# Kernel tuning notes

Measured on AMD Instinct MI355X. Metric: run time of the kernel, lower is better.

Reference implementation:

```python
import jax, jax.numpy as jnp
import numpy as np

EMB_DIM = 2048
USER_DIM = 256
NUM_EXPERTS = 64
TOP_K = 8
N_TOKENS = 16384


def setup_inputs() -> dict:
    key = jax.random.key(0)
    k_h, k_u, k_w = jax.random.split(key, 3)
    h = jax.random.normal(k_h, (N_TOKENS, EMB_DIM), dtype=jnp.float32)
    u = jax.random.normal(k_u, (N_TOKENS, USER_DIM), dtype=jnp.float32)
    # nn.Linear weight is [out, in]; we store transposed [in, out] for x @ W
    W = jax.random.normal(k_w, (EMB_DIM + USER_DIM, NUM_EXPERTS), dtype=jnp.float32) * (1.0 / np.sqrt(EMB_DIM + USER_DIM))
    b = jnp.zeros((NUM_EXPERTS,), dtype=jnp.float32)
    return {"h": h, "u": u, "W": W, "b": b}


def reference(h, u, W, b):
    # gate logits: [N, E]
    g = jnp.concatenate([h, u], axis=-1) @ W + b
    w = jax.nn.softmax(g, axis=-1)
    # top-k mask + renormalize (top_k < num_experts)
    _, top_idx = jax.lax.top_k(w, TOP_K)                       # [N, k]
    mask = jax.nn.one_hot(top_idx, NUM_EXPERTS, dtype=w.dtype).sum(axis=-2)  # [N, E]
    w = w * mask
    w = w / (w.sum(axis=-1, keepdims=True) + 1e-9)
    return w
```

## Files before the change

kernel.cpp:

```cpp
#include <hip/hip_runtime.h>

#define EMB 2048
#define UDIM 256
#define KTOT 2304
#define NE 64
#define TOPK 8
#define TPB 64
#define LP 65
#define BK 64
#define NWIN (KTOT / BK)
#define ESL 16

__global__ __launch_bounds__(1024, 4)
void gate_fused(const float* __restrict__ h, const float* __restrict__ u,
                const float* __restrict__ W, const float* __restrict__ b,
                float* __restrict__ out) {
  __shared__ float xt[2][TPB * LP];

  const int tid = threadIdx.x;
  const int lane = tid & 63;
  const int wid = __builtin_amdgcn_readfirstlane(tid >> 6);
  const int kq = wid & 3;
  const int ew = wid >> 2;
  const int tok0 = blockIdx.x * TPB;

  const int stok = tid >> 4;
  const int sseg = (tid & 15) * 4;

  float acc[ESL];
#pragma unroll
  for (int j = 0; j < ESL; ++j) acc[j] = 0.f;

  {
    float4 v = *(const float4*)(h + (size_t)(tok0 + stok) * EMB + sseg);
    float* dst = &xt[0][stok * LP + sseg];
    dst[0] = v.x; dst[1] = v.y; dst[2] = v.z; dst[3] = v.w;
  }
  __syncthreads();

  const int xbase = lane * LP + kq * 16;
  int p = 0;
  for (int w = 0; w < NWIN; ++w) {
    float4 v;
    if (w + 1 < NWIN) {
      const int kn = (w + 1) * BK;
      const float* src = (kn < EMB)
          ? h + (size_t)(tok0 + stok) * EMB + kn + sseg
          : u + (size_t)(tok0 + stok) * UDIM + (kn - EMB) + sseg;
      v = *(const float4*)src;
    }

    const float* wp = W + (size_t)(w * BK + kq * 16) * NE + ew * ESL;
    const float* xp = &xt[p][xbase];

    float4 wc[2][4];
#pragma unroll
    for (int kk = 0; kk < 2; ++kk)
#pragma unroll
      for (int j = 0; j < 4; ++j)
        wc[kk][j] = *(const float4*)(wp + kk * NE + 4 * j);

#pragma unroll
    for (int pr = 0; pr < 8; ++pr) {
      float4 wn[2][4];
      if (pr < 7) {
        const float* wq = wp + (size_t)(2 * pr + 2) * NE;
#pragma unroll
        for (int kk = 0; kk < 2; ++kk)
#pragma unroll
          for (int j = 0; j < 4; ++j)
            wn[kk][j] = *(const float4*)(wq + kk * NE + 4 * j);
      }
      const float x0 = xp[2 * pr];
      const float x1 = xp[2 * pr + 1];
#pragma unroll
      for (int j = 0; j < 4; ++j) {
        acc[4 * j + 0] = __builtin_fmaf(x0, wc[0][j].x, acc[4 * j + 0]);
        acc[4 * j + 1] = __builtin_fmaf(x0, wc[0][j].y, acc[4 * j + 1]);
        acc[4 * j + 2] = __builtin_fmaf(x0, wc[0][j].z, acc[4 * j + 2]);
        acc[4 * j + 3] = __builtin_fmaf(x0, wc[0][j].w, acc[4 * j + 3]);
      }
#pragma unroll
      for (int j = 0; j < 4; ++j) {
        acc[4 * j + 0] = __builtin_fmaf(x1, wc[1][j].x, acc[4 * j + 0]);
        acc[4 * j + 1] = __builtin_fmaf(x1, wc[1][j].y, acc[4 * j + 1]);
        acc[4 * j + 2] = __builtin_fmaf(x1, wc[1][j].z, acc[4 * j + 2]);
        acc[4 * j + 3] = __builtin_fmaf(x1, wc[1][j].w, acc[4 * j + 3]);
      }
      if (pr < 7) {
#pragma unroll
        for (int kk = 0; kk < 2; ++kk)
#pragma unroll
          for (int j = 0; j < 4; ++j) wc[kk][j] = wn[kk][j];
      }
    }

    if (w + 1 < NWIN) {
      float* dst = &xt[1 - p][stok * LP + sseg];
      dst[0] = v.x; dst[1] = v.y; dst[2] = v.z; dst[3] = v.w;
    }
    __syncthreads();
    p ^= 1;
  }

  float* slab = xt[0];
  for (int ph = 0; ph < 4; ++ph) {
    if (kq == ph) {
      float* srow = slab + lane * LP + ew * ESL;
      if (ph == 0) {
#pragma unroll
        for (int j = 0; j < ESL; ++j) srow[j] = acc[j];
      } else {
#pragma unroll
        for (int j = 0; j < ESL; ++j) srow[j] += acc[j];
      }
    }
    __syncthreads();
  }

  const float bias = b[lane];
#pragma unroll
  for (int tt = 0; tt < 4; ++tt) {
    const int t = wid * 4 + tt;
    float g = slab[t * LP + lane] + bias;

    float m = g;
#pragma unroll
    for (int off = 32; off > 0; off >>= 1)
      m = fmaxf(m, __shfl_xor(m, off));
    float pexp = __expf(g - m);
    float s = pexp;
#pragma unroll
    for (int off = 32; off > 0; off >>= 1)
      s += __shfl_xor(s, off);
    const float pn = pexp / s;

    float vv = pn;
    float topsum = 0.f;
    int sel = 0;
    for (int r = 0; r < TOPK; ++r) {
      float mv = vv;
      int mi = lane;
#pragma unroll
      for (int off = 32; off > 0; off >>= 1) {
        const float ov = __shfl_xor(mv, off);
        const int oi = __shfl_xor(mi, off);
        if (ov > mv || (ov == mv && oi < mi)) { mv = ov; mi = oi; }
      }
      topsum += mv;
      if (lane == mi) { sel = 1; vv = -1.f; }
    }

    out[(size_t)(tok0 + t) * NE + lane] =
        sel ? pn / (topsum + 1e-9f) : 0.f;
  }
}

extern "C" void kernel_launch(void* const* d_in, const int* in_sizes, int n_in,
                              void* d_out, int out_size, void* d_ws, size_t ws_size,
                              hipStream_t stream) {
  const float* h = (const float*)d_in[0];
  const float* u = (const float*)d_in[1];
  const float* W = (const float*)d_in[2];
  const float* b = (const float*)d_in[3];
  float* out = (float*)d_out;

  const int n_tokens = in_sizes[0] / EMB;
  const int n_blocks = n_tokens / TPB;

  hipLaunchKernelGGL(gate_fused, dim3(n_blocks), dim3(1024), 0, stream,
                     h, u, W, b, out);
}
```

Before: 293.8 us.

## Replace FP32 FMA gate GEMM with split-bf16 MFMA emulation

```diff
diff --git a/kernel.cpp b/kernel.cpp
--- a/kernel.cpp
+++ b/kernel.cpp
@@ -5,115 +5,138 @@
 #define KTOT 2304
 #define NE 64
 #define TOPK 8
-#define TPB 64
+#define TPB 32
 #define LP 65
-#define BK 64
-#define NWIN (KTOT / BK)
-#define ESL 16
+#define PLANE (KTOT * NE)
 
-__global__ __launch_bounds__(1024, 4)
-void gate_fused(const float* __restrict__ h, const float* __restrict__ u,
-                const float* __restrict__ W, const float* __restrict__ b,
-                float* __restrict__ out) {
-  __shared__ float xt[2][TPB * LP];
+typedef __attribute__((ext_vector_type(8))) short short8;
+typedef __attribute__((ext_vector_type(4))) float f32x4;
+
+__device__ __forceinline__ unsigned short bf16h(float x) {
+  unsigned uu = __builtin_bit_cast(unsigned, x);
+  return (unsigned short)((uu + 0x7FFFu + ((uu >> 16) & 1u)) >> 16);
+}
+__device__ __forceinline__ float bf2f(unsigned short s) {
+  return __builtin_bit_cast(float, ((unsigned)s) << 16);
+}
+
+__global__ __launch_bounds__(256)
+void prep_w(const float* __restrict__ W, unsigned short* __restrict__ wt) {
+  __shared__ unsigned short t0[64][72], t1[64][72], t2[64][72];
+  const int t = threadIdx.x;
+  const int kb = blockIdx.x * 64;
+#pragma unroll
+  for (int i = 0; i < 16; ++i) {
+    const int flat = i * 256 + t;
+    const int kk = flat >> 6;
+    const int nn = flat & 63;
+    const float w = W[(size_t)(kb + kk) * NE + nn];
+    const unsigned short h0 = bf16h(w);
+    const float r1 = w - bf2f(h0);
+    const unsigned short h1 = bf16h(r1);
+    const float r2 = r1 - bf2f(h1);
+    t0[nn][kk] = h0;
+    t1[nn][kk] = h1;
+    t2[nn][kk] = bf16h(r2);
+  }
+  __syncthreads();
+#pragma unroll
+  for (int i = 0; i < 16; ++i) {
+    const int flat = i * 256 + t;
+    const int nn = flat >> 6;
+    const int kk = flat & 63;
+    const size_t idx = (size_t)nn * KTOT + kb + kk;
+    wt[idx] = t0[nn][kk];
+    wt[PLANE + idx] = t1[nn][kk];
+    wt[2 * PLANE + idx] = t2[nn][kk];
+  }
+}
+
+__global__ __launch_bounds__(512, 4)
+void gate_mfma(const float* __restrict__ h, const float* __restrict__ u,
+               const unsigned short* __restrict__ wt,
+               const float* __restrict__ b, float* __restrict__ out) {
+  __shared__ float slab[TPB * LP];
 
   const int tid = threadIdx.x;
   const int lane = tid & 63;
   const int wid = __builtin_amdgcn_readfirstlane(tid >> 6);
-  const int kq = wid & 3;
-  const int ew = wid >> 2;
+  const int tw = wid & 1;
+  const int kq = wid >> 1;
+  const int mm = lane & 15;
+  const int q8 = (lane >> 4) * 8;
   const int tok0 = blockIdx.x * TPB;
+  const int token = tok0 + tw * 16 + mm;
 
-  const int stok = tid >> 4;
-  const int sseg = (tid & 15) * 4;
+  const float* hrow = h + (size_t)token * EMB + q8;
+  const float* urow = u + (size_t)token * UDIM + q8;
+  const unsigned short* wrow[4];
+#pragma unroll
+  for (int nt = 0; nt < 4; ++nt)
+    wrow[nt] = wt + (size_t)(nt * 16 + mm) * KTOT + q8;
 
-  float acc[ESL];
+  f32x4 acc[4];
 #pragma unroll
-  for (int j = 0; j < ESL; ++j) acc[j] = 0.f;
+  for (int nt = 0; nt < 4; ++nt) acc[nt] = 0.f;
 
-  {
-    float4 v = *(const float4*)(h + (size_t)(tok0 + stok) * EMB + sseg);
-    float* dst = &xt[0][stok * LP + sseg];
-    dst[0] = v.x; dst[1] = v.y; dst[2] = v.z; dst[3] = v.w;
-  }
-  __syncthreads();
-
-  const int xbase = lane * LP + kq * 16;
-  int p = 0;
-  for (int w = 0; w < NWIN; ++w) {
-    float4 v;
-    if (w + 1 < NWIN) {
-      const int kn = (w + 1) * BK;
-      const float* src = (kn < EMB)
-          ? h + (size_t)(tok0 + stok) * EMB + kn + sseg
-          : u + (size_t)(tok0 + stok) * UDIM + (kn - EMB) + sseg;
-      v = *(const float4*)src;
-    }
-
-    const float* wp = W + (size_t)(w * BK + kq * 16) * NE + ew * ESL;
-    const float* xp = &xt[p][xbase];
-
-    float4 wc[2][4];
+  auto run = [&](const float* __restrict__ xp, int kw0, int nsteps) {
+    f32x4 a0 = *(const f32x4*)(xp);
+    f32x4 a1 = *(const f32x4*)(xp + 4);
+    for (int s = 0; s < nsteps; ++s) {
+      f32x4 p0 = 0.f, p1 = 0.f;
+      if (s + 1 < nsteps) {
+        p0 = *(const f32x4*)(xp + (s + 1) * 32);
+        p1 = *(const f32x4*)(xp + (s + 1) * 32 + 4);
+      }
+      const int kw = kw0 + s * 32;
+      float xs[8] = {a0[0], a0[1], a0[2], a0[3], a1[0], a1[1], a1[2], a1[3]};
+      short8 A0, A1, A2;
 #pragma unroll
-    for (int kk = 0; kk < 2; ++kk)
-#pragma unroll
-      for (int j = 0; j < 4; ++j)
-        wc[kk][j] = *(const float4*)(wp + kk * NE + 4 * j);
-
-#pragma unroll
-    for (int pr = 0; pr < 8; ++pr) {
-      float4 wn[2][4];
-      if (pr < 7) {
-        const float* wq = wp + (size_t)(2 * pr + 2) * NE;
-#pragma unroll
-        for (int kk = 0; kk < 2; ++kk)
-#pragma unroll
-          for (int j = 0; j < 4; ++j)
-            wn[kk][j] = *(const float4*)(wq + kk * NE + 4 * j);
-      }
-      const float x0 = xp[2 * pr];
-      const float x1 = xp[2 * pr + 1];
-#pragma unroll
-      for (int j = 0; j < 4; ++j) {
-        acc[4 * j + 0] = __builtin_fmaf(x0, wc[0][j].x, acc[4 * j + 0]);
-        acc[4 * j + 1] = __builtin_fmaf(x0, wc[0][j].y, acc[4 * j + 1]);
-        acc[4 * j + 2] = __builtin_fmaf(x0, wc[0][j].z, acc[4 * j + 2]);
-        acc[4 * j + 3] = __builtin_fmaf(x0, wc[0][j].w, acc[4 * j + 3]);
+      for (int j = 0; j < 8; ++j) {
+        const unsigned short h0 = bf16h(xs[j]);
+        const float r1 = xs[j] - bf2f(h0);
+        const unsigned short h1 = bf16h(r1);
+        const float r2 = r1 - bf2f(h1);
+        A0[j] = (short)h0;
+        A1[j] = (short)h1;
+        A2[j] = (short)bf16h(r2);
       }
 #pragma unroll
-      for (int j = 0; j < 4; ++j) {
-        acc[4 * j + 0] = __builtin_fmaf(x1, wc[1][j].x, acc[4 * j + 0]);
-        acc[4 * j + 1] = __builtin_fmaf(x1, wc[1][j].y, acc[4 * j + 1]);
-        acc[4 * j + 2] = __builtin_fmaf(x1, wc[1][j].z, acc[4 * j + 2]);
-        acc[4 * j + 3] = __builtin_fmaf(x1, wc[1][j].w, acc[4 * j + 3]);
+      for (int nt = 0; nt < 4; ++nt) {
+        const unsigned short* wp = wrow[nt] + kw;
+        const short8 B0 = *(const short8*)(wp);
+        const short8 B1 = *(const short8*)(wp + PLANE);
+        const short8 B2 = *(const short8*)(wp + 2 * PLANE);
+        acc[nt] = __builtin_amdgcn_mfma_f32_16x16x32_bf16(A0, B0, acc[nt], 0, 0, 0);
+        acc[nt] = __builtin_amdgcn_mfma_f32_16x16x32_bf16(A0, B1, acc[nt], 0, 0, 0);
+        acc[nt] = __builtin_amdgcn_mfma_f32_16x16x32_bf16(A1, B0, acc[nt], 0, 0, 0);
+        acc[nt] = __builtin_amdgcn_mfma_f32_16x16x32_bf16(A1, B1, acc[nt], 0, 0, 0);
+        acc[nt] = __builtin_amdgcn_mfma_f32_16x16x32_bf16(A0, B2, acc[nt], 0, 0, 0);
+        acc[nt] = __builtin_amdgcn_mfma_f32_16x16x32_bf16(A2, B0, acc[nt], 0, 0, 0);
       }
-      if (pr < 7) {
-#pragma unroll
-        for (int kk = 0; kk < 2; ++kk)
-#pragma unroll
-          for (int j = 0; j < 4; ++j) wc[kk][j] = wn[kk][j];
-      }
+      a0 = p0;
+      a1 = p1;
     }
+  };
 
-    if (w + 1 < NWIN) {
-      float* dst = &xt[1 - p][stok * LP + sseg];
-      dst[0] = v.x; dst[1] = v.y; dst[2] = v.z; dst[3] = v.w;
-    }
-    __syncthreads();
-    p ^= 1;
+  const int kw0 = kq * 576;
+  if (kq < 3) {
+    run(hrow + kw0, kw0, 18);
+  } else {
+    run(hrow + 1728, 1728, 10);
+    run(urow, 2048, 8);
   }
 
-  float* slab = xt[0];
+  const int row = tw * 16 + (lane >> 4) * 4;
   for (int ph = 0; ph < 4; ++ph) {
     if (kq == ph) {
-      float* srow = slab + lane * LP + ew * ESL;
-      if (ph == 0) {
 #pragma unroll
-        for (int j = 0; j < ESL; ++j) srow[j] = acc[j];
-      } else {
+      for (int nt = 0; nt < 4; ++nt)
 #pragma unroll
-        for (int j = 0; j < ESL; ++j) srow[j] += acc[j];
-      }
+        for (int r = 0; r < 4; ++r) {
+          float* p = &slab[(row + r) * LP + nt * 16 + mm];
+          if (ph == 0) *p = acc[nt][r]; else *p += acc[nt][r];
+        }
     }
     __syncthreads();
   }
@@ -165,9 +188,11 @@
   const float* b = (const float*)d_in[3];
   float* out = (float*)d_out;
 
+  unsigned short* wt = (unsigned short*)d_ws;
+
   const int n_tokens = in_sizes[0] / EMB;
-  const int n_blocks = n_tokens / TPB;
 
-  hipLaunchKernelGGL(gate_fused, dim3(n_blocks), dim3(1024), 0, stream,
-                     h, u, W, b, out);
+  hipLaunchKernelGGL(prep_w, dim3(KTOT / 64), dim3(256), 0, stream, W, wt);
+  hipLaunchKernelGGL(gate_mfma, dim3(n_tokens / TPB), dim3(512), 0, stream,
+                     h, u, wt, b, out);
 }
```

After: 315.7 us. 1.07x slower.
